# Kernel tuning notes

Hardware: AMD Instinct MI355X
Metric: run time of the kernel (lower is better)

The kernel has to match this reference:

```python
import jax, jax.numpy as jnp
import numpy as np

N = 50000
E = 800000
IN_CH = 128
OUT_CH = 128
HEADS = 4
HEAD_DIM = OUT_CH // HEADS  # 32
NEG_SLOPE = 0.2
BN_EPS = 1e-5


def setup_inputs() -> dict:
    key = jax.random.key(0)
    ks = jax.random.split(key, 12)
    s = 1.0 / np.sqrt(IN_CH)
    x = jax.random.normal(ks[0], (N, IN_CH), dtype=jnp.float32)
    edge_index = jax.random.randint(ks[1], (2, E), 0, N, dtype=jnp.int64)
    # GATv2 lin_l (source) and lin_r (target) weights + biases
    W_l = jax.random.uniform(ks[2], (IN_CH, HEADS * HEAD_DIM), jnp.float32, -s, s)
    b_l = jax.random.uniform(ks[3], (HEADS * HEAD_DIM,), jnp.float32, -s, s)
    W_r = jax.random.uniform(ks[4], (IN_CH, HEADS * HEAD_DIM), jnp.float32, -s, s)
    b_r = jax.random.uniform(ks[5], (HEADS * HEAD_DIM,), jnp.float32, -s, s)
    att = jax.random.uniform(ks[6], (HEADS, HEAD_DIM), jnp.float32, -s, s)
    bias = jnp.zeros((HEADS * HEAD_DIM,), jnp.float32)
    gamma = jnp.ones((OUT_CH,), jnp.float32)
    beta = jnp.zeros((OUT_CH,), jnp.float32)
    return {"x": x, "edge_index": edge_index, "W_l": W_l, "b_l": b_l,
            "W_r": W_r, "b_r": b_r, "att": att, "bias": bias,
            "gamma": gamma, "beta": beta}


def gatv2_layer(x, edge_index, W_l, b_l, W_r, b_r, att, bias, gamma, beta):
    # transformed source/target features: [N, H, C]
    x_l = (x @ W_l + b_l).reshape(N, HEADS, HEAD_DIM)
    x_r = (x @ W_r + b_r).reshape(N, HEADS, HEAD_DIM)
    # add self loops
    loop = jnp.arange(N, dtype=edge_index.dtype)
    src = jnp.concatenate([edge_index[0], loop])
    dst = jnp.concatenate([edge_index[1], loop])
    # GATv2 attention scores per edge: a^T LeakyReLU(x_j + x_i)  -> [Etot, H]
    e = jax.nn.leaky_relu(x_l[src] + x_r[dst], NEG_SLOPE)
    score = jnp.einsum('ehc,hc->eh', e, att)
    # segment softmax over incoming edges of each destination node
    m = jax.ops.segment_max(score, dst, num_segments=N)
    ex = jnp.exp(score - m[dst])
    denom = jax.ops.segment_sum(ex, dst, num_segments=N)
    alpha = ex / denom[dst]
    # scatter-add aggregation of alpha * x_l[src]
    out = jax.ops.segment_sum(alpha[:, :, None] * x_l[src], dst, num_segments=N)
    out = out.reshape(N, OUT_CH) + bias
    # BatchNorm over nodes (training-mode batch statistics)
    mu = jnp.mean(out, axis=0)
    var = jnp.var(out, axis=0)
    out = (out - mu) / jnp.sqrt(var + BN_EPS) * gamma + beta
    # residual (in_channels == out_channels -> identity path) + ELU
    out = jax.nn.elu(out + x)
    return out


def reference(x, edge_index, W_l, b_l, W_r, b_r, att, bias, gamma, beta):
    return gatv2_layer(x, edge_index, W_l, b_l, W_r, b_r, att, bias, gamma, beta)
```

## Files before the change

kernel.cpp:

```cpp
#include <hip/hip_runtime.h>

#define NN 50000
#define EE 800000
#define ETOT (EE + NN)
#define GEMM_BLOCKS 1563
#define COUNT_BLOCKS 3125
#define SCAN_BLOCKS 196

__device__ __forceinline__ unsigned bf16r(float f) {
  unsigned u = __float_as_uint(f);
  return (u + 0x7FFFu + ((u >> 16) & 1u)) >> 16;
}

__device__ __forceinline__ float4 unpack_bf16x4(unsigned a, unsigned b) {
  float4 f;
  f.x = __uint_as_float(a << 16);
  f.y = __uint_as_float(a & 0xFFFF0000u);
  f.z = __uint_as_float(b << 16);
  f.w = __uint_as_float(b & 0xFFFF0000u);
  return f;
}

__global__ __launch_bounds__(256) void gemm_count(
    const float* __restrict__ x,
    const float* __restrict__ Wl, const float* __restrict__ bl,
    const float* __restrict__ Wr, const float* __restrict__ br,
    unsigned short* __restrict__ xlh, float* __restrict__ xr,
    const int* __restrict__ ei, int* __restrict__ deg) {
  __shared__ float xs[32][132];
  __shared__ float wt[16][264];
  if (blockIdx.x >= GEMM_BLOCKS) {
    int e = (blockIdx.x - GEMM_BLOCKS) * 256 + threadIdx.x;
    if (e < EE) atomicAdd(&deg[ei[EE + e]], 1);
    return;
  }
  const int t = threadIdx.x;
  const int tx = t & 31, ty = t >> 5;
  const int bnode = blockIdx.x * 32;

#pragma unroll
  for (int i = 0; i < 4; ++i) {
    int idx = t + i * 256;
    int node = idx >> 5, f4 = idx & 31;
    int gn = bnode + node;
    float4 v = make_float4(0.f, 0.f, 0.f, 0.f);
    if (gn < NN) v = *(const float4*)&x[(size_t)gn * 128 + f4 * 4];
    *(float4*)&xs[node][f4 * 4] = v;
  }
  __syncthreads();

  float acc[2][4][4];
#pragma unroll
  for (int m = 0; m < 2; ++m)
#pragma unroll
    for (int n = 0; n < 4; ++n)
#pragma unroll
      for (int j = 0; j < 4; ++j) acc[m][n][j] = 0.f;

  for (int kt = 0; kt < 8; ++kt) {
    if (kt) __syncthreads();
#pragma unroll
    for (int i = 0; i < 4; ++i) {
      int idx = t + i * 256;
      int kk = idx >> 6, g = idx & 63;
      int krow = kt * 16 + kk;
      const float* s = (g < 32) ? &Wl[krow * 128 + g * 4]
                                : &Wr[krow * 128 + (g - 32) * 4];
      *(float4*)&wt[kk][g * 4] = *(const float4*)s;
    }
    __syncthreads();
#pragma unroll
    for (int kk4 = 0; kk4 < 4; ++kk4) {
      float xa[4][4];
#pragma unroll
      for (int n = 0; n < 4; ++n)
        *(float4*)&xa[n][0] = *(const float4*)&xs[ty * 4 + n][kt * 16 + kk4 * 4];
#pragma unroll
      for (int q = 0; q < 4; ++q) {
        float4 wl4 = *(const float4*)&wt[kk4 * 4 + q][tx * 4];
        float4 wr4 = *(const float4*)&wt[kk4 * 4 + q][128 + tx * 4];
        float wl_[4] = {wl4.x, wl4.y, wl4.z, wl4.w};
        float wr_[4] = {wr4.x, wr4.y, wr4.z, wr4.w};
#pragma unroll
        for (int n = 0; n < 4; ++n) {
          float xv = xa[n][q];
#pragma unroll
          for (int j = 0; j < 4; ++j) {
            acc[0][n][j] = fmaf(xv, wl_[j], acc[0][n][j]);
            acc[1][n][j] = fmaf(xv, wr_[j], acc[1][n][j]);
          }
        }
      }
    }
  }

  float4 bl4 = *(const float4*)&bl[tx * 4];
  float4 br4 = *(const float4*)&br[tx * 4];
#pragma unroll
  for (int n = 0; n < 4; ++n) {
    int gn = bnode + ty * 4 + n;
    if (gn < NN) {
      float ox = acc[0][n][0] + bl4.x, oy = acc[0][n][1] + bl4.y;
      float oz = acc[0][n][2] + bl4.z, ow = acc[0][n][3] + bl4.w;
      uint2 hv;
      hv.x = bf16r(ox) | (bf16r(oy) << 16);
      hv.y = bf16r(oz) | (bf16r(ow) << 16);
      *(uint2*)(xlh + (size_t)gn * 128 + tx * 4) = hv;
      float4 o;
      o.x = acc[1][n][0] + br4.x; o.y = acc[1][n][1] + br4.y;
      o.z = acc[1][n][2] + br4.z; o.w = acc[1][n][3] + br4.w;
      *(float4*)&xr[(size_t)gn * 128 + tx * 4] = o;
    }
  }
}

__global__ __launch_bounds__(256) void scanA(const int* __restrict__ deg,
                                             int* __restrict__ bsum,
                                             float* __restrict__ bn) {
  __shared__ int s[256];
  int t = threadIdx.x;
  if (blockIdx.x == 0) bn[t] = 0.f;
  int i = blockIdx.x * 256 + t;
  s[t] = (i < NN) ? deg[i] : 0;
  __syncthreads();
#pragma unroll
  for (int off = 128; off > 0; off >>= 1) {
    if (t < off) s[t] += s[t + off];
    __syncthreads();
  }
  if (t == 0) bsum[blockIdx.x] = s[0];
}

__global__ __launch_bounds__(256) void scanB(const int* __restrict__ deg,
                                             const int* __restrict__ bsum,
                                             int* __restrict__ offs,
                                             int* __restrict__ cursor) {
  __shared__ int s[256];
  __shared__ int bpref;
  int t = threadIdx.x;
  int bid = blockIdx.x;
  int i = bid * 256 + t;
  int v = (i < NN) ? deg[i] : 0;
  s[t] = v;
  if (t == 0) {
    int r = 0;
    for (int k = 0; k < bid; ++k) r += bsum[k];
    bpref = r;
  }
  __syncthreads();
  for (int off = 1; off < 256; off <<= 1) {
    int u = (t >= off) ? s[t - off] : 0;
    __syncthreads();
    s[t] += u;
    __syncthreads();
  }
  int excl = s[t] - v + bpref;
  if (i <= NN) {
    offs[i] = excl;
    if (i < NN) cursor[i] = excl;
  }
}

__global__ void fill_csr(const int* __restrict__ ei, int* __restrict__ cursor,
                         int* __restrict__ csr) {
  int e = blockIdx.x * 256 + threadIdx.x;
  if (e >= ETOT) return;
  int s, d;
  if (e < EE) { s = ei[e]; d = ei[EE + e]; }
  else { s = e - EE; d = s; }
  int pos = atomicAdd(&cursor[d], 1);
  csr[pos] = s;
}

__global__ __launch_bounds__(256) void aggregate(
    const unsigned short* __restrict__ xlh, const float* __restrict__ xr,
    const int* __restrict__ offs, const int* __restrict__ csr,
    const float* __restrict__ att,
    float* __restrict__ out, float* __restrict__ bn) {
  __shared__ float sbn[256];
  int t = threadIdx.x;
  sbn[t] = 0.f;
  __syncthreads();
  const int lane = t & 63;
  const int gl = lane & 15;
  const int gb = lane & 48;
  const int c8 = gl * 8;
  const int gid = (blockIdx.x * 256 + t) >> 4;
  const int gstride = gridDim.x * 16;
  const float4 at0 = *(const float4*)&att[c8];
  const float4 at1 = *(const float4*)&att[c8 + 4];
  float4 bs0 = make_float4(0, 0, 0, 0), bs1 = make_float4(0, 0, 0, 0);
  float4 bq0 = make_float4(0, 0, 0, 0), bq1 = make_float4(0, 0, 0, 0);

  for (int node = gid; node < NN; node += gstride) {
    const float4 xr0 = *(const float4*)&xr[(size_t)node * 128 + c8];
    const float4 xr1 = *(const float4*)&xr[(size_t)node * 128 + c8 + 4];
    const int beg = offs[node];
    const int deg = offs[node + 1] - beg;
    float den = 0.f;
    float4 a0 = make_float4(0, 0, 0, 0), a1 = make_float4(0, 0, 0, 0);

    for (int base = 0; base < deg; base += 16) {
      int cnt = deg - base; if (cnt > 16) cnt = 16;
      int msrc = (gl < cnt) ? csr[beg + base + gl] : 0;
      for (int eb = 0; eb < cnt; eb += 8) {
        uint4 u[8];
#pragma unroll
        for (int j = 0; j < 8; ++j) {
          int s = __shfl(msrc, gb + eb + j, 64);
          u[j] = *(const uint4*)(xlh + (size_t)s * 128 + c8);
        }
#pragma unroll
        for (int j = 0; j < 8; ++j) {
          float4 v0 = unpack_bf16x4(u[j].x, u[j].y);
          float4 v1 = unpack_bf16x4(u[j].z, u[j].w);
          float e, p;
          e = v0.x + xr0.x; e = e > 0.f ? e : 0.2f * e; p = e * at0.x;
          e = v0.y + xr0.y; e = e > 0.f ? e : 0.2f * e; p = fmaf(e, at0.y, p);
          e = v0.z + xr0.z; e = e > 0.f ? e : 0.2f * e; p = fmaf(e, at0.z, p);
          e = v0.w + xr0.w; e = e > 0.f ? e : 0.2f * e; p = fmaf(e, at0.w, p);
          e = v1.x + xr1.x; e = e > 0.f ? e : 0.2f * e; p = fmaf(e, at1.x, p);
          e = v1.y + xr1.y; e = e > 0.f ? e : 0.2f * e; p = fmaf(e, at1.y, p);
          e = v1.z + xr1.z; e = e > 0.f ? e : 0.2f * e; p = fmaf(e, at1.z, p);
          e = v1.w + xr1.w; e = e > 0.f ? e : 0.2f * e; p = fmaf(e, at1.w, p);
          p += __shfl_xor(p, 1);
          p += __shfl_xor(p, 2);
          float pe = (eb + j < cnt) ? __expf(p) : 0.f;
          den += pe;
          a0.x = fmaf(pe, v0.x, a0.x);
          a0.y = fmaf(pe, v0.y, a0.y);
          a0.z = fmaf(pe, v0.z, a0.z);
          a0.w = fmaf(pe, v0.w, a0.w);
          a1.x = fmaf(pe, v1.x, a1.x);
          a1.y = fmaf(pe, v1.y, a1.y);
          a1.z = fmaf(pe, v1.z, a1.z);
          a1.w = fmaf(pe, v1.w, a1.w);
        }
      }
    }

    float inv = 1.0f / den;
    float4 r0, r1;
    r0.x = a0.x * inv; r0.y = a0.y * inv; r0.z = a0.z * inv; r0.w = a0.w * inv;
    r1.x = a1.x * inv; r1.y = a1.y * inv; r1.z = a1.z * inv; r1.w = a1.w * inv;
    *(float4*)&out[(size_t)node * 128 + c8] = r0;
    *(float4*)&out[(size_t)node * 128 + c8 + 4] = r1;
    bs0.x += r0.x; bs0.y += r0.y; bs0.z += r0.z; bs0.w += r0.w;
    bs1.x += r1.x; bs1.y += r1.y; bs1.z += r1.z; bs1.w += r1.w;
    bq0.x += r0.x * r0.x; bq0.y += r0.y * r0.y; bq0.z += r0.z * r0.z; bq0.w += r0.w * r0.w;
    bq1.x += r1.x * r1.x; bq1.y += r1.y * r1.y; bq1.z += r1.z * r1.z; bq1.w += r1.w * r1.w;
  }

#define RED(F) F = F + __shfl_xor(F, 16); F = F + __shfl_xor(F, 32);
  RED(bs0.x) RED(bs0.y) RED(bs0.z) RED(bs0.w)
  RED(bs1.x) RED(bs1.y) RED(bs1.z) RED(bs1.w)
  RED(bq0.x) RED(bq0.y) RED(bq0.z) RED(bq0.w)
  RED(bq1.x) RED(bq1.y) RED(bq1.z) RED(bq1.w)
#undef RED
  if (lane < 16) {
    atomicAdd(&sbn[c8 + 0], bs0.x);
    atomicAdd(&sbn[c8 + 1], bs0.y);
    atomicAdd(&sbn[c8 + 2], bs0.z);
    atomicAdd(&sbn[c8 + 3], bs0.w);
    atomicAdd(&sbn[c8 + 4], bs1.x);
    atomicAdd(&sbn[c8 + 5], bs1.y);
    atomicAdd(&sbn[c8 + 6], bs1.z);
    atomicAdd(&sbn[c8 + 7], bs1.w);
    atomicAdd(&sbn[128 + c8 + 0], bq0.x);
    atomicAdd(&sbn[128 + c8 + 1], bq0.y);
    atomicAdd(&sbn[128 + c8 + 2], bq0.z);
    atomicAdd(&sbn[128 + c8 + 3], bq0.w);
    atomicAdd(&sbn[128 + c8 + 4], bq1.x);
    atomicAdd(&sbn[128 + c8 + 5], bq1.y);
    atomicAdd(&sbn[128 + c8 + 6], bq1.z);
    atomicAdd(&sbn[128 + c8 + 7], bq1.w);
  }
  __syncthreads();
  atomicAdd(&bn[t], sbn[t]);
}

__global__ __launch_bounds__(256) void finalize(
    float* __restrict__ out, const float* __restrict__ x,
    const float* __restrict__ bn, const float* __restrict__ gamma,
    const float* __restrict__ beta) {
  __shared__ float smu[128], sgi[128];
  int t = threadIdx.x;
  if (t < 128) {
    float mu = bn[t] * (1.0f / NN);
    float var = bn[128 + t] * (1.0f / NN) - mu * mu;
    smu[t] = mu;
    sgi[t] = rsqrtf(var + 1e-5f) * gamma[t];
  }
  __syncthreads();
  const int total4 = NN * 32;
  for (int i = blockIdx.x * blockDim.x + threadIdx.x; i < total4;
       i += gridDim.x * blockDim.x) {
    int c4 = (i & 31) * 4;
    float4 o = ((const float4*)out)[i];
    float4 xv = ((const float4*)x)[i];
    float4 mu = *(const float4*)&smu[c4];
    float4 gi = *(const float4*)&sgi[c4];
    float4 b4 = *(const float4*)&beta[c4];
    float v;
    v = (o.x - mu.x) * gi.x + b4.x + xv.x; o.x = v > 0.f ? v : expm1f(v);
    v = (o.y - mu.y) * gi.y + b4.y + xv.y; o.y = v > 0.f ? v : expm1f(v);
    v = (o.z - mu.z) * gi.z + b4.z + xv.z; o.z = v > 0.f ? v : expm1f(v);
    v = (o.w - mu.w) * gi.w + b4.w + xv.w; o.w = v > 0.f ? v : expm1f(v);
    ((float4*)out)[i] = o;
  }
}

extern "C" void kernel_launch(void* const* d_in, const int* in_sizes, int n_in,
                              void* d_out, int out_size, void* d_ws, size_t ws_size,
                              hipStream_t stream) {
  const float* x    = (const float*)d_in[0];
  const int*   ei   = (const int*)d_in[1];
  const float* Wl   = (const float*)d_in[2];
  const float* bl   = (const float*)d_in[3];
  const float* Wr   = (const float*)d_in[4];
  const float* br   = (const float*)d_in[5];
  const float* att  = (const float*)d_in[6];
  const float* gam  = (const float*)d_in[8];
  const float* bet  = (const float*)d_in[9];
  float* out = (float*)d_out;

  unsigned short* xlh = (unsigned short*)d_ws;
  float* xr   = (float*)(xlh + (size_t)NN * 128);
  int* offs   = (int*)(xr + (size_t)NN * 128);
  int* cursor = offs + (NN + 4);
  int* deg    = cursor + NN;
  int* csr    = deg + NN;
  float* bn   = (float*)(csr + ETOT);
  int* bsum   = (int*)(bn + 256);

  hipMemsetD32Async((hipDeviceptr_t)deg, 1, NN, stream);

  hipLaunchKernelGGL(gemm_count, dim3(GEMM_BLOCKS + COUNT_BLOCKS), dim3(256), 0,
                     stream, x, Wl, bl, Wr, br, xlh, xr, ei, deg);
  hipLaunchKernelGGL(scanA, dim3(SCAN_BLOCKS), dim3(256), 0, stream, deg, bsum, bn);
  hipLaunchKernelGGL(scanB, dim3(SCAN_BLOCKS), dim3(256), 0, stream,
                     deg, bsum, offs, cursor);
  hipLaunchKernelGGL(fill_csr, dim3((ETOT + 255) / 256), dim3(256), 0, stream,
                     ei, cursor, csr);
  hipLaunchKernelGGL(aggregate, dim3(GEMM_BLOCKS), dim3(256), 0, stream,
                     xlh, xr, offs, csr, att, out, bn);
  hipLaunchKernelGGL(finalize, dim3(2048), dim3(256), 0, stream, out, x, bn, gam, bet);
}
```

Before: 348.6 us.

## Replace FP32 LDS-tiled projection GEMM with bf16 MFMA persistent kernel

Rewrites the fused x@[W_l|W_r] projection to use MFMA 16x16x32 bf16 instructions. Weights are converted to bf16 and kept in registers per wave, and a persistent grid of 512 blocks loops over 64-row tiles. Input rows are read straight from global memory and rounded to bf16, removing LDS staging and the scalar FMA loop. The trade-off is lower precision for x and the weights, plus scalar strided output stores and strided weight loads per block.

```diff
diff --git a/kernel.cpp b/kernel.cpp
--- a/kernel.cpp
+++ b/kernel.cpp
@@ -3,9 +3,14 @@
 #define NN 50000
 #define EE 800000
 #define ETOT (EE + NN)
-#define GEMM_BLOCKS 1563
+#define GEMM_GRID 512
+#define MTILES 782
 #define COUNT_BLOCKS 3125
+#define AGG_BLOCKS 1563
 #define SCAN_BLOCKS 196
+
+typedef __attribute__((ext_vector_type(8))) short bhalf8;
+typedef __attribute__((ext_vector_type(4))) float fx4;
 
 __device__ __forceinline__ unsigned bf16r(float f) {
   unsigned u = __float_as_uint(f);
@@ -27,89 +32,80 @@
     const float* __restrict__ Wr, const float* __restrict__ br,
     unsigned short* __restrict__ xlh, float* __restrict__ xr,
     const int* __restrict__ ei, int* __restrict__ deg) {
-  __shared__ float xs[32][132];
-  __shared__ float wt[16][264];
-  if (blockIdx.x >= GEMM_BLOCKS) {
-    int e = (blockIdx.x - GEMM_BLOCKS) * 256 + threadIdx.x;
+  if (blockIdx.x >= GEMM_GRID) {
+    int e = (blockIdx.x - GEMM_GRID) * 256 + threadIdx.x;
     if (e < EE) atomicAdd(&deg[ei[EE + e]], 1);
     return;
   }
   const int t = threadIdx.x;
-  const int tx = t & 31, ty = t >> 5;
-  const int bnode = blockIdx.x * 32;
-
-#pragma unroll
-  for (int i = 0; i < 4; ++i) {
-    int idx = t + i * 256;
-    int node = idx >> 5, f4 = idx & 31;
-    int gn = bnode + node;
-    float4 v = make_float4(0.f, 0.f, 0.f, 0.f);
-    if (gn < NN) v = *(const float4*)&x[(size_t)gn * 128 + f4 * 4];
-    *(float4*)&xs[node][f4 * 4] = v;
-  }
-  __syncthreads();
-
-  float acc[2][4][4];
-#pragma unroll
-  for (int m = 0; m < 2; ++m)
-#pragma unroll
-    for (int n = 0; n < 4; ++n)
-#pragma unroll
-      for (int j = 0; j < 4; ++j) acc[m][n][j] = 0.f;
-
-  for (int kt = 0; kt < 8; ++kt) {
-    if (kt) __syncthreads();
-#pragma unroll
-    for (int i = 0; i < 4; ++i) {
-      int idx = t + i * 256;
-      int kk = idx >> 6, g = idx & 63;
-      int krow = kt * 16 + kk;
-      const float* s = (g < 32) ? &Wl[krow * 128 + g * 4]
-                                : &Wr[krow * 128 + (g - 32) * 4];
-      *(float4*)&wt[kk][g * 4] = *(const float4*)s;
+  const int w = t >> 6;
+  const int l = t & 63;
+  const int cl = l & 15;
+  const int kb = (l >> 4) * 8;
+  const int rsub = (l >> 4) * 4;
+
+  bhalf8 bfr[4][4];
+  float biasv[4];
+#pragma unroll
+  for (int nt = 0; nt < 4; ++nt) {
+    int col = w * 64 + nt * 16 + cl;
+    const float* Wsrc;
+    if (col < 128) { Wsrc = Wl + col; biasv[nt] = bl[col]; }
+    else           { Wsrc = Wr + (col - 128); biasv[nt] = br[col - 128]; }
+#pragma unroll
+    for (int ch = 0; ch < 4; ++ch) {
+      int k0 = ch * 32 + kb;
+      bhalf8 f;
+#pragma unroll
+      for (int j = 0; j < 8; ++j)
+        f[j] = (short)bf16r(Wsrc[(size_t)(k0 + j) * 128]);
+      bfr[nt][ch] = f;
     }
-    __syncthreads();
-#pragma unroll
-    for (int kk4 = 0; kk4 < 4; ++kk4) {
-      float xa[4][4];
-#pragma unroll
-      for (int n = 0; n < 4; ++n)
-        *(float4*)&xa[n][0] = *(const float4*)&xs[ty * 4 + n][kt * 16 + kk4 * 4];
-#pragma unroll
-      for (int q = 0; q < 4; ++q) {
-        float4 wl4 = *(const float4*)&wt[kk4 * 4 + q][tx * 4];
-        float4 wr4 = *(const float4*)&wt[kk4 * 4 + q][128 + tx * 4];
-        float wl_[4] = {wl4.x, wl4.y, wl4.z, wl4.w};
-        float wr_[4] = {wr4.x, wr4.y, wr4.z, wr4.w};
-#pragma unroll
-        for (int n = 0; n < 4; ++n) {
-          float xv = xa[n][q];
-#pragma unroll
-          for (int j = 0; j < 4; ++j) {
-            acc[0][n][j] = fmaf(xv, wl_[j], acc[0][n][j]);
-            acc[1][n][j] = fmaf(xv, wr_[j], acc[1][n][j]);
+  }
+
+  for (int mt = blockIdx.x; mt < MTILES; mt += GEMM_GRID) {
+    const int m0 = mt * 64;
+#pragma unroll
+    for (int rt = 0; rt < 4; ++rt) {
+      int row = m0 + rt * 16 + cl;
+      int rowc = row < NN ? row : NN - 1;
+      const float* xp = x + (size_t)rowc * 128 + kb;
+      bhalf8 afr[4];
+#pragma unroll
+      for (int ch = 0; ch < 4; ++ch) {
+        float4 q0 = *(const float4*)(xp + ch * 32);
+        float4 q1 = *(const float4*)(xp + ch * 32 + 4);
+        bhalf8 f;
+        f[0] = (short)bf16r(q0.x); f[1] = (short)bf16r(q0.y);
+        f[2] = (short)bf16r(q0.z); f[3] = (short)bf16r(q0.w);
+        f[4] = (short)bf16r(q1.x); f[5] = (short)bf16r(q1.y);
+        f[6] = (short)bf16r(q1.z); f[7] = (short)bf16r(q1.w);
+        afr[ch] = f;
+      }
+#pragma unroll
+      for (int nt = 0; nt < 4; ++nt) {
+        fx4 acc = {biasv[nt], biasv[nt], biasv[nt], biasv[nt]};
+#pragma unroll
+        for (int ch = 0; ch < 4; ++ch)
+          acc = __builtin_amdgcn_mfma_f32_16x16x32_bf16(afr[ch], bfr[nt][ch],
+                                                        acc, 0, 0, 0);
+        int col = w * 64 + nt * 16 + cl;
+        int rbase = m0 + rt * 16 + rsub;
+        if (col < 128) {
+#pragma unroll
+          for (int r = 0; r < 4; ++r) {
+            int rr = rbase + r;
+            if (rr < NN) xlh[(size_t)rr * 128 + col] = (unsigned short)bf16r(acc[r]);
+          }
+        } else {
+          int c2 = col - 128;
+#pragma unroll
+          for (int r = 0; r < 4; ++r) {
+            int rr = rbase + r;
+            if (rr < NN) xr[(size_t)rr * 128 + c2] = acc[r];
           }
         }
       }
-    }
-  }
-
-  float4 bl4 = *(const float4*)&bl[tx * 4];
-  float4 br4 = *(const float4*)&br[tx * 4];
-#pragma unroll
-  for (int n = 0; n < 4; ++n) {
-    int gn = bnode + ty * 4 + n;
-    if (gn < NN) {
-      float ox = acc[0][n][0] + bl4.x, oy = acc[0][n][1] + bl4.y;
-      float oz = acc[0][n][2] + bl4.z, ow = acc[0][n][3] + bl4.w;
-      uint2 hv;
-      hv.x = bf16r(ox) | (bf16r(oy) << 16);
-      hv.y = bf16r(oz) | (bf16r(ow) << 16);
-      *(uint2*)(xlh + (size_t)gn * 128 + tx * 4) = hv;
-      float4 o;
-      o.x = acc[1][n][0] + br4.x; o.y = acc[1][n][1] + br4.y;
-      o.z = acc[1][n][2] + br4.z; o.w = acc[1][n][3] + br4.w;
-      *(float4*)&xr[(size_t)gn * 128 + tx * 4] = o;
     }
   }
 }
@@ -335,14 +331,14 @@
 
   hipMemsetD32Async((hipDeviceptr_t)deg, 1, NN, stream);
 
-  hipLaunchKernelGGL(gemm_count, dim3(GEMM_BLOCKS + COUNT_BLOCKS), dim3(256), 0,
+  hipLaunchKernelGGL(gemm_count, dim3(GEMM_GRID + COUNT_BLOCKS), dim3(256), 0,
                      stream, x, Wl, bl, Wr, br, xlh, xr, ei, deg);
   hipLaunchKernelGGL(scanA, dim3(SCAN_BLOCKS), dim3(256), 0, stream, deg, bsum, bn);
   hipLaunchKernelGGL(scanB, dim3(SCAN_BLOCKS), dim3(256), 0, stream,
                      deg, bsum, offs, cursor);
   hipLaunchKernelGGL(fill_csr, dim3((ETOT + 255) / 256), dim3(256), 0, stream,
                      ei, cursor, csr);
-  hipLaunchKernelGGL(aggregate, dim3(GEMM_BLOCKS), dim3(256), 0, stream,
+  hipLaunchKernelGGL(aggregate, dim3(AGG_BLOCKS), dim3(256), 0, stream,
                      xlh, xr, offs, csr, att, out, bn);
   hipLaunchKernelGGL(finalize, dim3(2048), dim3(256), 0, stream, out, x, bn, gam, bet);
 }
```

New measurement: 298.8 us. 1.17x faster.
